# Optimization experiments

Hardware: AMD Instinct MI355X
Metric: run time of the kernel (lower is better)

The kernel has to match this reference:

```python
import jax, jax.numpy as jnp
import numpy as np

SEQ_LEN = 256
NLAYERS = 3
H = 128  # latent_dim == input_dim
OUT_DIM = 2
BATCH = 1024


def setup_inputs() -> dict:
    key = jax.random.key(0)
    ks = jax.random.split(key, 7)
    s = 1.0 / np.sqrt(H)  # PyTorch RNN init scale
    return {
        "hiddens": jax.random.normal(ks[0], (BATCH, NLAYERS, H), jnp.float32),
        "W_ih": jax.random.uniform(ks[1], (NLAYERS, 3 * H, H), jnp.float32, -s, s),
        "W_hh": jax.random.uniform(ks[2], (NLAYERS, 3 * H, H), jnp.float32, -s, s),
        "b_ih": jax.random.uniform(ks[3], (NLAYERS, 3 * H), jnp.float32, -s, s),
        "b_hh": jax.random.uniform(ks[4], (NLAYERS, 3 * H), jnp.float32, -s, s),
        "fc_w": jax.random.uniform(ks[5], (OUT_DIM, H), jnp.float32, -s, s),
        "fc_b": jax.random.uniform(ks[6], (OUT_DIM,), jnp.float32, -s, s),
    }


def _gru_cell(x, h, w_ih, w_hh, bi, bh):
    # x, h: [B, H]; w_*: [3H, H]; b_*: [3H]; PyTorch gate order (r, z, n)
    gx = x @ w_ih.T + bi          # [B, 3H]
    gh = h @ w_hh.T + bh          # [B, 3H]
    xr, xz, xn = jnp.split(gx, 3, axis=-1)
    hr, hz, hn = jnp.split(gh, 3, axis=-1)
    r = jax.nn.sigmoid(xr + hr)
    z = jax.nn.sigmoid(xz + hz)
    n = jnp.tanh(xn + r * hn)
    return (1.0 - z) * n + z * h


def reference(hiddens, W_ih, W_hh, b_ih, b_hh, fc_w, fc_b):
    # hiddens: [B, L, H] -> layer-major [L, B, H] (torch transposes 0,1)
    h = jnp.transpose(hiddens, (1, 0, 2))
    B = hiddens.shape[0]
    x0 = jnp.zeros((B, H), hiddens.dtype)  # torch.zeros initial input

    def step(carry, _):
        x, h = carry
        new_h = []
        inp = x
        for l in range(NLAYERS):
            hl = _gru_cell(inp, h[l], W_ih[l], W_hh[l], b_ih[l], b_hh[l])
            new_h.append(hl)
            inp = hl  # top-layer output feeds next layer / next step
        return (inp, jnp.stack(new_h)), inp

    (_, _), outs = jax.lax.scan(step, (x0, h), None, length=SEQ_LEN)
    outs = jnp.transpose(outs, (1, 0, 2))        # [B, T, H]
    return outs @ fc_w.T + fc_b                  # [B, T, out_dim]
```

## Files before the change

### kernel.cpp

```cpp
#include <hip/hip_runtime.h>
#include <stdint.h>

typedef int   v4i __attribute__((ext_vector_type(4)));
typedef float v4f __attribute__((ext_vector_type(4)));

#define SLOT_SZ  13824
#define LO_OFF   6912
#define BIAS_OFF (2*SLOT_SZ)
#define FC_OFF   (BIAS_OFF + 6144)
#define SMEM_SZ  (FC_OFF + 2048)

#define QW   1436.84056f
#define C1f  4.38394754e-5f
#define C2f  3.45193507e-7f
#define L2E  1.44269504f
#define CR1  (-(L2E)*C1f)
#define CR2  (-(L2E)*C2f)
#define CX1  (2.0f*L2E*C1f)
#define CX2  (2.0f*L2E*C2f)

#define MFMA(A,B,C) __builtin_amdgcn_mfma_i32_16x16x64_i8(A, B, C, 0, 0, 0)

__global__ void prep_weights(const float* __restrict__ Wih,
                             const float* __restrict__ Whh,
                             int8_t* __restrict__ img) {
  int bid = blockIdx.x, lane = threadIdx.x;
  int w = bid / 36, blk = bid % 36;
  int l = blk / 12, rem = blk % 12, o = rem >> 1, kh = rem & 1;
  const float* M = (o & 1) ? Whh : Wih;
  int row = (o >> 1) * 128 + w * 16 + (lane & 15);
  int k0 = kh * 64 + (lane >> 4) * 16;
  const float* src = M + l * 49152 + row * 128 + k0;
  int words[4];
  #pragma unroll
  for (int j4 = 0; j4 < 4; ++j4) {
    unsigned wd = 0;
    #pragma unroll
    for (int j = 0; j < 4; ++j) {
      int q = (int)rintf(src[j4 * 4 + j] * QW);
      wd |= ((unsigned)(q & 255)) << (8 * j);
    }
    words[j4] = (int)wd;
  }
  *(v4i*)(img + (((long)bid) * 64 + lane) * 16) = *(const v4i*)words;
}

__global__ __launch_bounds__(512, 2)
void gru_main(const float* __restrict__ hiddens, const float* __restrict__ bih,
              const float* __restrict__ bhh, const float* __restrict__ fcw,
              const float* __restrict__ fcb, const int8_t* __restrict__ img,
              float* __restrict__ out) {
  extern __shared__ char smem[];
  const int tid = threadIdx.x, wg = blockIdx.x;
  const int lane = tid & 63, w = tid >> 6, col = lane & 15, q = lane >> 4;

  v4i wr[36];
  #pragma unroll
  for (int i = 0; i < 36; ++i)
    wr[i] = *(const v4i*)(img + (((long)(w * 36 + i)) * 64 + lane) * 16);

  if (tid < 128) {
    int kh = tid >> 6, ln = tid & 63, c2 = ln & 15, q2 = ln >> 4;
    int words[4] = {0, 0, 0, 0};
    if (c2 < 2) {
      const float* src = fcw + c2 * 128 + kh * 64 + q2 * 16;
      #pragma unroll
      for (int j4 = 0; j4 < 4; ++j4) {
        unsigned wd = 0;
        #pragma unroll
        for (int j = 0; j < 4; ++j) {
          int qv = (int)rintf(src[j4 * 4 + j] * QW);
          wd |= ((unsigned)(qv & 255)) << (8 * j);
        }
        words[j4] = (int)wd;
      }
    }
    *(v4i*)(smem + FC_OFF + kh * 1024 + ln * 16) = *(const v4i*)words;
  }
  for (int i = tid; i < 1536; i += 512) {
    int l = i >> 9, type = (i >> 7) & 3, h = i & 127;
    float bv;
    if      (type == 0) bv = -L2E * (bih[l * 384 + h]       + bhh[l * 384 + h]);
    else if (type == 1) bv = -L2E * (bih[l * 384 + 128 + h] + bhh[l * 384 + 128 + h]);
    else if (type == 2) bv = 2.0f * L2E * bih[l * 384 + 256 + h];
    else                bv = 2.0f * L2E * bhh[l * 384 + 256 + h];
    *(float*)(smem + BIAS_OFF + i * 4) = bv;
  }
  for (int i = tid; i < 6144; i += 512) {
    int l = i >> 11, b = (i >> 7) & 15, h = i & 127;
    float v = hiddens[((long)(wg * 16 + b)) * 384 + l * 128 + h];
    float f = v * 15.875f, fhi = rintf(f);
    *(int8_t*)(smem + l * 2304 + b * 144 + h)          = (int8_t)(int)fhi;
    *(int8_t*)(smem + l * 2304 + b * 144 + h + LO_OFF) = (int8_t)(int)rintf((f - fhi) * 127.f);
  }
  v4f hst[3];
  #pragma unroll
  for (int l = 0; l < 3; ++l)
    #pragma unroll
    for (int r = 0; r < 4; ++r)
      hst[l][r] = hiddens[((long)(wg * 16 + col)) * 384 + l * 128 + w * 16 + q * 4 + r];

  const float fcb0 = fcb[0], fcb1 = fcb[1];
  __syncthreads();

  const char* fragb = smem + col * 144 + q * 16;
  char* ewb = smem + col * 144 + w * 16 + q * 4;
  const char* biasb = smem + BIAS_OFF + (w * 16 + q * 4) * 4;

  v4i c2h[2], c2l[2];

  #pragma unroll 1
  for (int t = 0; t < 256; ++t) {
    const int so = (t & 1) * SLOT_SZ;
    const int sn = SLOT_SZ - so;
    #pragma unroll
    for (int l = 0; l < 3; ++l) {
      v4f bRv = *(const v4f*)(biasb + (l * 4 + 0) * 512);
      v4f bZv = *(const v4f*)(biasb + (l * 4 + 1) * 512);
      v4f bXv = *(const v4f*)(biasb + (l * 4 + 2) * 512);
      v4f bHv = *(const v4f*)(biasb + (l * 4 + 3) * 512);
      v4i aRh = {0,0,0,0}, aRl = {0,0,0,0}, aZh = {0,0,0,0}, aZl = {0,0,0,0};
      v4i aXh = {0,0,0,0}, aXl = {0,0,0,0}, aHh = {0,0,0,0}, aHl = {0,0,0,0};
      if (l > 0 || t > 0) {
        #pragma unroll
        for (int kh = 0; kh < 2; ++kh) {
          v4i xh, xl;
          if (l == 0) {
            xh = *(const v4i*)(fragb + so + 2 * 2304 + kh * 64);
            xl = *(const v4i*)(fragb + so + 2 * 2304 + kh * 64 + LO_OFF);
            c2h[kh] = xh; c2l[kh] = xl;
          } else {
            xh = *(const v4i*)(fragb + sn + (l - 1) * 2304 + kh * 64);
            xl = *(const v4i*)(fragb + sn + (l - 1) * 2304 + kh * 64 + LO_OFF);
          }
          aRh = MFMA(wr[l*12 + 0 + kh], xh, aRh);
          aRl = MFMA(wr[l*12 + 0 + kh], xl, aRl);
          aZh = MFMA(wr[l*12 + 4 + kh], xh, aZh);
          aZl = MFMA(wr[l*12 + 4 + kh], xl, aZl);
          aXh = MFMA(wr[l*12 + 8 + kh], xh, aXh);
          aXl = MFMA(wr[l*12 + 8 + kh], xl, aXl);
        }
      }
      #pragma unroll
      for (int kh = 0; kh < 2; ++kh) {
        v4i hh, hl;
        if (l == 2) {
          if (t == 0) { c2h[kh] = *(const v4i*)(fragb + so + 2 * 2304 + kh * 64);
                        c2l[kh] = *(const v4i*)(fragb + so + 2 * 2304 + kh * 64 + LO_OFF); }
          hh = c2h[kh]; hl = c2l[kh];
        } else {
          hh = *(const v4i*)(fragb + so + l * 2304 + kh * 64);
          hl = *(const v4i*)(fragb + so + l * 2304 + kh * 64 + LO_OFF);
        }
        aRh = MFMA(wr[l*12 + 2 + kh], hh, aRh);
        aRl = MFMA(wr[l*12 + 2 + kh], hl, aRl);
        aZh = MFMA(wr[l*12 + 6 + kh], hh, aZh);
        aZl = MFMA(wr[l*12 + 6 + kh], hl, aZl);
        aHh = MFMA(wr[l*12 + 10 + kh], hh, aHh);
        aHl = MFMA(wr[l*12 + 10 + kh], hl, aHl);
      }
      unsigned hiw = 0, low = 0;
      #pragma unroll
      for (int r = 0; r < 4; ++r) {
        float gR = fmaf(CR1, (float)aRh[r], fmaf(CR2, (float)aRl[r], bRv[r]));
        float gZ = fmaf(CR1, (float)aZh[r], fmaf(CR2, (float)aZl[r], bZv[r]));
        float gX = fmaf(CX1, (float)aXh[r], fmaf(CX2, (float)aXl[r], bXv[r]));
        float gH = fmaf(CX1, (float)aHh[r], fmaf(CX2, (float)aHl[r], bHv[r]));
        float rg = __builtin_amdgcn_rcpf(1.f + __builtin_amdgcn_exp2f(gR));
        float zg = __builtin_amdgcn_rcpf(1.f + __builtin_amdgcn_exp2f(gZ));
        float u  = __builtin_amdgcn_rcpf(1.f + __builtin_amdgcn_exp2f(fmaf(rg, gH, gX)));
        float ng = fmaf(-2.f, u, 1.f);
        float hn = fmaf(zg, hst[l][r] - ng, ng);
        hst[l][r] = hn;
        float f = hn * 15.875f, fhi = rintf(f);
        hiw |= ((unsigned)(((int)fhi) & 255)) << (8 * r);
        low |= ((unsigned)(((int)rintf((f - fhi) * 127.f)) & 255)) << (8 * r);
      }
      *(unsigned*)(ewb + sn + l * 2304)          = hiw;
      *(unsigned*)(ewb + sn + l * 2304 + LO_OFF) = low;
      __syncthreads();
    }
    if (w == 0) {
      v4i dh = {0,0,0,0}, dl = {0,0,0,0};
      #pragma unroll
      for (int kh = 0; kh < 2; ++kh) {
        v4i xh = *(const v4i*)(fragb + sn + 2 * 2304 + kh * 64);
        v4i xl = *(const v4i*)(fragb + sn + 2 * 2304 + kh * 64 + LO_OFF);
        v4i fw = *(const v4i*)(smem + FC_OFF + kh * 1024 + lane * 16);
        dh = MFMA(fw, xh, dh);
        dl = MFMA(fw, xl, dl);
      }
      if (q == 0) {
        float2 o2;
        o2.x = fcb0 + C1f * (float)dh[0] + C2f * (float)dl[0];
        o2.y = fcb1 + C1f * (float)dh[1] + C2f * (float)dl[1];
        *(float2*)(out + (((long)(wg * 16 + col)) * 256 + t) * 2) = o2;
      }
    }
  }
}

extern "C" void kernel_launch(void* const* d_in, const int* in_sizes, int n_in,
                              void* d_out, int out_size, void* d_ws, size_t ws_size,
                              hipStream_t stream) {
  (void)in_sizes; (void)n_in; (void)out_size; (void)ws_size;
  const float* hiddens = (const float*)d_in[0];
  const float* Wih     = (const float*)d_in[1];
  const float* Whh     = (const float*)d_in[2];
  const float* bih     = (const float*)d_in[3];
  const float* bhh     = (const float*)d_in[4];
  const float* fcw     = (const float*)d_in[5];
  const float* fcb     = (const float*)d_in[6];
  int8_t* img = (int8_t*)d_ws;
  float* out = (float*)d_out;

  prep_weights<<<288, 64, 0, stream>>>(Wih, Whh, img);
  gru_main<<<64, 512, SMEM_SZ, stream>>>(hiddens, bih, bhh, fcw, fcb, img, out);
}
```

Baseline: 839.1 us.

## Split GRU layers across wave groups with wavefront pipelining and LDS weight spill

Waves 0-3 now own layers 0 and 2, and waves 4-7 own layer 1. Each wave handles two output tiles, and the hidden-state matmul parts of the next layer are computed ahead while the other group finishes, so each timestep has three barriers with overlapped work instead of three fully serial layer phases. Part of the weights no longer fits in registers and moves to a larger LDS region. The int8 hi/lo split is changed to one combined scale so the two accumulators merge with a shift. The FC projection moves to wave 4 and runs one step behind. The price is extra LDS weight reads each step, larger shared memory, and less parallelism per layer, since only 4 waves work on each layer.

```diff
diff --git a/kernel.cpp b/kernel.cpp
--- a/kernel.cpp
+++ b/kernel.cpp
@@ -8,16 +8,15 @@
 #define LO_OFF   6912
 #define BIAS_OFF (2*SLOT_SZ)
 #define FC_OFF   (BIAS_OFF + 6144)
-#define SMEM_SZ  (FC_OFF + 2048)
+#define WLDS_A   (FC_OFF + 2048)
+#define WLDS_B   (WLDS_A + 81920)
+#define SMEM_SZ  (WLDS_B + 16384)
 
 #define QW   1436.84056f
-#define C1f  4.38394754e-5f
-#define C2f  3.45193507e-7f
 #define L2E  1.44269504f
-#define CR1  (-(L2E)*C1f)
-#define CR2  (-(L2E)*C2f)
-#define CX1  (2.0f*L2E*C1f)
-#define CX2  (2.0f*L2E*C2f)
+#define CMf  (1.0f/(QW*2032.0f))
+#define CRmf (-(L2E)*CMf)
+#define CXmf (2.0f*(L2E)*CMf)
 
 #define MFMA(A,B,C) __builtin_amdgcn_mfma_i32_16x16x64_i8(A, B, C, 0, 0, 0)
 
@@ -53,12 +52,38 @@
   extern __shared__ char smem[];
   const int tid = threadIdx.x, wg = blockIdx.x;
   const int lane = tid & 63, w = tid >> 6, col = lane & 15, q = lane >> 4;
-
-  v4i wr[36];
-  #pragma unroll
-  for (int i = 0; i < 36; ++i)
-    wr[i] = *(const v4i*)(img + (((long)(w * 36 + i)) * 64 + lane) * 16);
-
+  const bool isA = (w < 4);
+  const int g = isA ? w : (w - 4);
+
+#define LDIMG(BLK) (*(const v4i*)(img + (((long)(BLK)) * 64 + lane) * 16))
+#define LDSA(i,u)  (*(const v4i*)(smem + WLDS_A + g*20480 + ((i)*10+(u))*1024 + lane*16))
+#define LDSB(i,u)  (*(const v4i*)(smem + WLDS_B + g*4096  + ((i)*2 +(u))*1024 + lane*16))
+
+  v4i wra[2][14]; v4i wrb[2][10];
+  if (isA) {
+    #pragma unroll
+    for (int i = 0; i < 2; ++i) {
+      const int tw = (2 * g + i) * 36;
+      #pragma unroll
+      for (int k = 0; k < 10; ++k) wra[i][k] = LDIMG(tw + k);
+      wra[i][10] = LDIMG(tw + 26); wra[i][11] = LDIMG(tw + 27);
+      wra[i][12] = LDIMG(tw + 28); wra[i][13] = LDIMG(tw + 29);
+      const int blks[10] = {10, 11, 24, 25, 30, 31, 32, 33, 34, 35};
+      #pragma unroll
+      for (int u = 0; u < 10; ++u)
+        *(v4i*)(smem + WLDS_A + g*20480 + (i*10+u)*1024 + lane*16) = LDIMG(tw + blks[u]);
+    }
+  } else {
+    #pragma unroll
+    for (int i = 0; i < 2; ++i) {
+      const int tw = (2 * g + i) * 36;
+      #pragma unroll
+      for (int k = 0; k < 10; ++k) wrb[i][k] = LDIMG(tw + 12 + k);
+      #pragma unroll
+      for (int u = 0; u < 2; ++u)
+        *(v4i*)(smem + WLDS_B + g*4096 + (i*2+u)*1024 + lane*16) = LDIMG(tw + 22 + u);
+    }
+  }
   if (tid < 128) {
     int kh = tid >> 6, ln = tid & 63, c2 = ln & 15, q2 = ln >> 4;
     int words[4] = {0, 0, 0, 0};
@@ -89,113 +114,182 @@
   for (int i = tid; i < 6144; i += 512) {
     int l = i >> 11, b = (i >> 7) & 15, h = i & 127;
     float v = hiddens[((long)(wg * 16 + b)) * 384 + l * 128 + h];
-    float f = v * 15.875f, fhi = rintf(f);
-    *(int8_t*)(smem + l * 2304 + b * 144 + h)          = (int8_t)(int)fhi;
-    *(int8_t*)(smem + l * 2304 + b * 144 + h + LO_OFF) = (int8_t)(int)rintf((f - fhi) * 127.f);
-  }
-  v4f hst[3];
-  #pragma unroll
-  for (int l = 0; l < 3; ++l)
-    #pragma unroll
-    for (int r = 0; r < 4; ++r)
-      hst[l][r] = hiddens[((long)(wg * 16 + col)) * 384 + l * 128 + w * 16 + q * 4 + r];
-
+    int V = (int)rintf(v * 2032.f);
+    int hb = (V + 64) >> 7, lb = V - (hb << 7);
+    *(int8_t*)(smem + l * 2304 + b * 144 + h)          = (int8_t)hb;
+    *(int8_t*)(smem + l * 2304 + b * 144 + h + LO_OFF) = (int8_t)lb;
+  }
+  v4f hstA[2][2]; v4f hstB[2];
+  if (isA) {
+    #pragma unroll
+    for (int il = 0; il < 2; ++il)
+      #pragma unroll
+      for (int i = 0; i < 2; ++i)
+        #pragma unroll
+        for (int r = 0; r < 4; ++r)
+          hstA[il][i][r] = hiddens[((long)(wg*16+col))*384 + (il*2)*128 + (2*g+i)*16 + q*4 + r];
+  } else {
+    #pragma unroll
+    for (int i = 0; i < 2; ++i)
+      #pragma unroll
+      for (int r = 0; r < 4; ++r)
+        hstB[i][r] = hiddens[((long)(wg*16+col))*384 + 128 + (2*g+i)*16 + q*4 + r];
+  }
   const float fcb0 = fcb[0], fcb1 = fcb[1];
   __syncthreads();
 
+  v4i fcr0 = {0,0,0,0}, fcr1 = {0,0,0,0};
+  if (w == 4) {
+    fcr0 = *(const v4i*)(smem + FC_OFF + lane * 16);
+    fcr1 = *(const v4i*)(smem + FC_OFF + 1024 + lane * 16);
+  }
+
   const char* fragb = smem + col * 144 + q * 16;
-  char* ewb = smem + col * 144 + w * 16 + q * 4;
-  const char* biasb = smem + BIAS_OFF + (w * 16 + q * 4) * 4;
-
-  v4i c2h[2], c2l[2];
+
+  auto lda = [&](const char* ap, v4i* f) {
+    f[0] = *(const v4i*)ap;            f[1] = *(const v4i*)(ap + 64);
+    f[2] = *(const v4i*)(ap + LO_OFF); f[3] = *(const v4i*)(ap + LO_OFF + 64);
+  };
+  auto mm2 = [&](v4i& aH, v4i& aL, v4i w0, v4i w1, const v4i* p) {
+    aH = MFMA(w0, p[0], aH); aH = MFMA(w1, p[1], aH);
+    aL = MFMA(w0, p[2], aL); aL = MFMA(w1, p[3], aL);
+  };
+  auto ewt = [&](int L, int tile, v4i Rh, v4i Rl, v4i Zh, v4i Zl,
+                 v4i Xh, v4i Xl, v4i Hh, v4i Hl, v4f& hst, int sn) {
+    const char* bb = smem + BIAS_OFF + (tile * 16 + q * 4) * 4;
+    v4f bR = *(const v4f*)(bb + (L * 4 + 0) * 512);
+    v4f bZ = *(const v4f*)(bb + (L * 4 + 1) * 512);
+    v4f bX = *(const v4f*)(bb + (L * 4 + 2) * 512);
+    v4f bH = *(const v4f*)(bb + (L * 4 + 3) * 512);
+    unsigned hiw = 0, low = 0;
+    #pragma unroll
+    for (int r = 0; r < 4; ++r) {
+      float gR = fmaf(CRmf, (float)((Rh[r] << 7) + Rl[r]), bR[r]);
+      float gZ = fmaf(CRmf, (float)((Zh[r] << 7) + Zl[r]), bZ[r]);
+      float gX = fmaf(CXmf, (float)((Xh[r] << 7) + Xl[r]), bX[r]);
+      float gH = fmaf(CXmf, (float)((Hh[r] << 7) + Hl[r]), bH[r]);
+      float rg = __builtin_amdgcn_rcpf(1.f + __builtin_amdgcn_exp2f(gR));
+      float zg = __builtin_amdgcn_rcpf(1.f + __builtin_amdgcn_exp2f(gZ));
+      float u  = __builtin_amdgcn_rcpf(1.f + __builtin_amdgcn_exp2f(fmaf(rg, gH, gX)));
+      float ng = fmaf(-2.f, u, 1.f);
+      float hn = fmaf(zg, hst[r] - ng, ng);
+      hst[r] = hn;
+      int V = (int)rintf(hn * 2032.f);
+      int hb = (V + 64) >> 7, lb = V - (hb << 7);
+      hiw |= ((unsigned)(hb & 255)) << (8 * r);
+      low |= ((unsigned)(lb & 255)) << (8 * r);
+    }
+    char* wp = smem + sn + L * 2304 + col * 144 + tile * 16 + q * 4;
+    *(unsigned*)wp = hiw;
+    *(unsigned*)(wp + LO_OFF) = low;
+  };
+
+  v4i pRh[2], pRl[2], pZh[2], pZl[2], pHh[2], pHl[2];
+  const v4i Z4 = {0, 0, 0, 0};
 
   #pragma unroll 1
   for (int t = 0; t < 256; ++t) {
     const int so = (t & 1) * SLOT_SZ;
     const int sn = SLOT_SZ - so;
-    #pragma unroll
-    for (int l = 0; l < 3; ++l) {
-      v4f bRv = *(const v4f*)(biasb + (l * 4 + 0) * 512);
-      v4f bZv = *(const v4f*)(biasb + (l * 4 + 1) * 512);
-      v4f bXv = *(const v4f*)(biasb + (l * 4 + 2) * 512);
-      v4f bHv = *(const v4f*)(biasb + (l * 4 + 3) * 512);
-      v4i aRh = {0,0,0,0}, aRl = {0,0,0,0}, aZh = {0,0,0,0}, aZl = {0,0,0,0};
-      v4i aXh = {0,0,0,0}, aXl = {0,0,0,0}, aHh = {0,0,0,0}, aHl = {0,0,0,0};
-      if (l > 0 || t > 0) {
-        #pragma unroll
-        for (int kh = 0; kh < 2; ++kh) {
-          v4i xh, xl;
-          if (l == 0) {
-            xh = *(const v4i*)(fragb + so + 2 * 2304 + kh * 64);
-            xl = *(const v4i*)(fragb + so + 2 * 2304 + kh * 64 + LO_OFF);
-            c2h[kh] = xh; c2l[kh] = xl;
-          } else {
-            xh = *(const v4i*)(fragb + sn + (l - 1) * 2304 + kh * 64);
-            xl = *(const v4i*)(fragb + sn + (l - 1) * 2304 + kh * 64 + LO_OFF);
-          }
-          aRh = MFMA(wr[l*12 + 0 + kh], xh, aRh);
-          aRl = MFMA(wr[l*12 + 0 + kh], xl, aRl);
-          aZh = MFMA(wr[l*12 + 4 + kh], xh, aZh);
-          aZl = MFMA(wr[l*12 + 4 + kh], xl, aZl);
-          aXh = MFMA(wr[l*12 + 8 + kh], xh, aXh);
-          aXl = MFMA(wr[l*12 + 8 + kh], xl, aXl);
+    if (isA) {
+      v4i ha[4], xa[4];
+      lda(fragb + so, ha);
+      if (t > 0) lda(fragb + so + 2 * 2304, xa);
+      #pragma unroll
+      for (int i = 0; i < 2; ++i) {
+        v4i Rh = Z4, Rl = Z4, Zh = Z4, Zl = Z4, Xh = Z4, Xl = Z4, Hh = Z4, Hl = Z4;
+        mm2(Rh, Rl, wra[i][2], wra[i][3], ha);
+        mm2(Zh, Zl, wra[i][6], wra[i][7], ha);
+        mm2(Hh, Hl, LDSA(i, 0), LDSA(i, 1), ha);
+        if (t > 0) {
+          mm2(Rh, Rl, wra[i][0], wra[i][1], xa);
+          mm2(Zh, Zl, wra[i][4], wra[i][5], xa);
+          mm2(Xh, Xl, wra[i][8], wra[i][9], xa);
         }
-      }
-      #pragma unroll
-      for (int kh = 0; kh < 2; ++kh) {
-        v4i hh, hl;
-        if (l == 2) {
-          if (t == 0) { c2h[kh] = *(const v4i*)(fragb + so + 2 * 2304 + kh * 64);
-                        c2l[kh] = *(const v4i*)(fragb + so + 2 * 2304 + kh * 64 + LO_OFF); }
-          hh = c2h[kh]; hl = c2l[kh];
-        } else {
-          hh = *(const v4i*)(fragb + so + l * 2304 + kh * 64);
-          hl = *(const v4i*)(fragb + so + l * 2304 + kh * 64 + LO_OFF);
-        }
-        aRh = MFMA(wr[l*12 + 2 + kh], hh, aRh);
-        aRl = MFMA(wr[l*12 + 2 + kh], hl, aRl);
-        aZh = MFMA(wr[l*12 + 6 + kh], hh, aZh);
-        aZl = MFMA(wr[l*12 + 6 + kh], hl, aZl);
-        aHh = MFMA(wr[l*12 + 10 + kh], hh, aHh);
-        aHl = MFMA(wr[l*12 + 10 + kh], hl, aHl);
-      }
-      unsigned hiw = 0, low = 0;
-      #pragma unroll
-      for (int r = 0; r < 4; ++r) {
-        float gR = fmaf(CR1, (float)aRh[r], fmaf(CR2, (float)aRl[r], bRv[r]));
-        float gZ = fmaf(CR1, (float)aZh[r], fmaf(CR2, (float)aZl[r], bZv[r]));
-        float gX = fmaf(CX1, (float)aXh[r], fmaf(CX2, (float)aXl[r], bXv[r]));
-        float gH = fmaf(CX1, (float)aHh[r], fmaf(CX2, (float)aHl[r], bHv[r]));
-        float rg = __builtin_amdgcn_rcpf(1.f + __builtin_amdgcn_exp2f(gR));
-        float zg = __builtin_amdgcn_rcpf(1.f + __builtin_amdgcn_exp2f(gZ));
-        float u  = __builtin_amdgcn_rcpf(1.f + __builtin_amdgcn_exp2f(fmaf(rg, gH, gX)));
-        float ng = fmaf(-2.f, u, 1.f);
-        float hn = fmaf(zg, hst[l][r] - ng, ng);
-        hst[l][r] = hn;
-        float f = hn * 15.875f, fhi = rintf(f);
-        hiw |= ((unsigned)(((int)fhi) & 255)) << (8 * r);
-        low |= ((unsigned)(((int)rintf((f - fhi) * 127.f)) & 255)) << (8 * r);
-      }
-      *(unsigned*)(ewb + sn + l * 2304)          = hiw;
-      *(unsigned*)(ewb + sn + l * 2304 + LO_OFF) = low;
-      __syncthreads();
-    }
-    if (w == 0) {
-      v4i dh = {0,0,0,0}, dl = {0,0,0,0};
-      #pragma unroll
-      for (int kh = 0; kh < 2; ++kh) {
-        v4i xh = *(const v4i*)(fragb + sn + 2 * 2304 + kh * 64);
-        v4i xl = *(const v4i*)(fragb + sn + 2 * 2304 + kh * 64 + LO_OFF);
-        v4i fw = *(const v4i*)(smem + FC_OFF + kh * 1024 + lane * 16);
-        dh = MFMA(fw, xh, dh);
-        dl = MFMA(fw, xl, dl);
-      }
+        ewt(0, 2 * g + i, Rh, Rl, Zh, Zl, Xh, Xl, Hh, Hl, hstA[0][i], sn);
+      }
+    } else if (w == 4 && t > 0) {
+      v4i fa[4];
+      lda(fragb + so + 2 * 2304, fa);
+      v4i dh = Z4, dl = Z4;
+      dh = MFMA(fcr0, fa[0], dh); dh = MFMA(fcr1, fa[1], dh);
+      dl = MFMA(fcr0, fa[2], dl); dl = MFMA(fcr1, fa[3], dl);
       if (q == 0) {
         float2 o2;
-        o2.x = fcb0 + C1f * (float)dh[0] + C2f * (float)dl[0];
-        o2.y = fcb1 + C1f * (float)dh[1] + C2f * (float)dl[1];
-        *(float2*)(out + (((long)(wg * 16 + col)) * 256 + t) * 2) = o2;
-      }
+        o2.x = fcb0 + CMf * (float)((dh[0] << 7) + dl[0]);
+        o2.y = fcb1 + CMf * (float)((dh[1] << 7) + dl[1]);
+        *(float2*)(out + (((long)(wg * 16 + col)) * 256 + (t - 1)) * 2) = o2;
+      }
+    }
+    __syncthreads();
+    if (isA) {
+      v4i ha[4];
+      lda(fragb + so + 2 * 2304, ha);
+      #pragma unroll
+      for (int i = 0; i < 2; ++i) {
+        pRh[i] = Z4; pRl[i] = Z4; pZh[i] = Z4; pZl[i] = Z4; pHh[i] = Z4; pHl[i] = Z4;
+        mm2(pRh[i], pRl[i], wra[i][10], wra[i][11], ha);
+        mm2(pZh[i], pZl[i], LDSA(i, 4), LDSA(i, 5), ha);
+        mm2(pHh[i], pHl[i], LDSA(i, 8), LDSA(i, 9), ha);
+      }
+    } else {
+      v4i xa[4], ha[4];
+      lda(fragb + sn, xa);
+      if (t == 0) lda(fragb + 1 * 2304, ha);
+      #pragma unroll
+      for (int i = 0; i < 2; ++i) {
+        if (t == 0) {
+          pRh[i] = Z4; pRl[i] = Z4; pZh[i] = Z4; pZl[i] = Z4; pHh[i] = Z4; pHl[i] = Z4;
+          mm2(pRh[i], pRl[i], wrb[i][2], wrb[i][3], ha);
+          mm2(pZh[i], pZl[i], wrb[i][6], wrb[i][7], ha);
+          mm2(pHh[i], pHl[i], LDSB(i, 0), LDSB(i, 1), ha);
+        }
+        v4i Xh = Z4, Xl = Z4;
+        mm2(pRh[i], pRl[i], wrb[i][0], wrb[i][1], xa);
+        mm2(pZh[i], pZl[i], wrb[i][4], wrb[i][5], xa);
+        mm2(Xh, Xl, wrb[i][8], wrb[i][9], xa);
+        ewt(1, 2 * g + i, pRh[i], pRl[i], pZh[i], pZl[i], Xh, Xl, pHh[i], pHl[i],
+            hstB[i], sn);
+      }
+    }
+    __syncthreads();
+    if (isA) {
+      v4i xa[4];
+      lda(fragb + sn + 1 * 2304, xa);
+      #pragma unroll
+      for (int i = 0; i < 2; ++i) {
+        v4i Xh = Z4, Xl = Z4;
+        mm2(pRh[i], pRl[i], LDSA(i, 2), LDSA(i, 3), xa);
+        mm2(pZh[i], pZl[i], wra[i][12], wra[i][13], xa);
+        mm2(Xh, Xl, LDSA(i, 6), LDSA(i, 7), xa);
+        ewt(2, 2 * g + i, pRh[i], pRl[i], pZh[i], pZl[i], Xh, Xl, pHh[i], pHl[i],
+            hstA[1][i], sn);
+      }
+    } else {
+      v4i ha[4];
+      lda(fragb + sn + 1 * 2304, ha);
+      #pragma unroll
+      for (int i = 0; i < 2; ++i) {
+        pRh[i] = Z4; pRl[i] = Z4; pZh[i] = Z4; pZl[i] = Z4; pHh[i] = Z4; pHl[i] = Z4;
+        mm2(pRh[i], pRl[i], wrb[i][2], wrb[i][3], ha);
+        mm2(pZh[i], pZl[i], wrb[i][6], wrb[i][7], ha);
+        mm2(pHh[i], pHl[i], LDSB(i, 0), LDSB(i, 1), ha);
+      }
+    }
+    __syncthreads();
+  }
+
+  if (w == 4) {
+    v4i fa[4];
+    lda(fragb + 2 * 2304, fa);
+    v4i dh = Z4, dl = Z4;
+    dh = MFMA(fcr0, fa[0], dh); dh = MFMA(fcr1, fa[1], dh);
+    dl = MFMA(fcr0, fa[2], dl); dl = MFMA(fcr1, fa[3], dl);
+    if (q == 0) {
+      float2 o2;
+      o2.x = fcb0 + CMf * (float)((dh[0] << 7) + dl[0]);
+      o2.y = fcb1 + CMf * (float)((dh[1] << 7) + dl[1]);
+      *(float2*)(out + (((long)(wg * 16 + col)) * 256 + 255) * 2) = o2;
     }
   }
 }
@@ -214,6 +308,9 @@
   int8_t* img = (int8_t*)d_ws;
   float* out = (float*)d_out;
 
+  hipFuncSetAttribute(reinterpret_cast<const void*>(gru_main),
+                      hipFuncAttributeMaxDynamicSharedMemorySize, SMEM_SZ);
+
   prep_weights<<<288, 64, 0, stream>>>(Wih, Whh, img);
   gru_main<<<64, 512, SMEM_SZ, stream>>>(hiddens, bih, bhh, fcw, fcb, img, out);
 }
```

After: 1.686 ms. 101% more time.
